# Kernel optimization log

Measured on AMD Instinct MI355X. Metric: run time of the kernel, lower is better.

The kernel has to match this reference:

```python
import jax, jax.numpy as jnp
import numpy as np

D = 1024
H = 16
HD = D // H


def setup_inputs() -> dict:
    key = jax.random.key(0)
    ks = jax.random.split(key, 9)
    s = 1.0 / np.sqrt(D)
    inp = {
        "x": jax.random.normal(ks[0], (2, 2048, D), dtype=jnp.float32),
        "Wq": jax.random.uniform(ks[1], (D, D), jnp.float32, -s, s),
        "bq": jax.random.uniform(ks[2], (D,), jnp.float32, -s, s),
        "Wk": jax.random.uniform(ks[3], (D, D), jnp.float32, -s, s),
        "bk": jax.random.uniform(ks[4], (D,), jnp.float32, -s, s),
        "Wv": jax.random.uniform(ks[5], (D, D), jnp.float32, -s, s),
        "bv": jax.random.uniform(ks[6], (D,), jnp.float32, -s, s),
        "Wo": jax.random.uniform(ks[7], (D, D), jnp.float32, -s, s),
        "bo": jax.random.uniform(ks[8], (D,), jnp.float32, -s, s),
    }
    return inp


def reference(x, Wq, bq, Wk, bk, Wv, bv, Wo, bo):
    B, S, _ = x.shape
    scale = jnp.sqrt(jnp.asarray(HD, dtype=jnp.float32))
    # QKV projections, split into heads: [B, H, S, HD]
    def proj(W, b):
        y = jnp.einsum('bsd,de->bse', x, W) + b
        return y.reshape(B, S, H, HD).transpose(0, 2, 1, 3)
    Q, K, V = proj(Wq, bq), proj(Wk, bk), proj(Wv, bv)
    scores = jnp.einsum('bhqd,bhkd->bhqk', Q, K) / scale  # [B,H,S,S]
    attn = jax.nn.softmax(scores, axis=-1)
    ctx = jnp.einsum('bhqk,bhkd->bhqd', attn, V)
    ctx = ctx.transpose(0, 2, 1, 3).reshape(B, S, D)
    return jnp.einsum('bsd,de->bse', ctx, Wo) + bo
```

## Files before the change

kernel.cpp:

```cpp
#include <hip/hip_runtime.h>
#include <hip/hip_bf16.h>

typedef __attribute__((ext_vector_type(8))) short bf16x8;
typedef __attribute__((ext_vector_type(4))) float f32x4;

constexpr int Sc  = 2048;
constexpr int Dc  = 1024;
constexpr int Hc  = 16;
constexpr int HDc = 64;
constexpr int Mc  = 4096;

constexpr float ECs = 0.18033688011112042f;

__device__ __forceinline__ ushort f2bf(float f) {
  unsigned u = __float_as_uint(f);
  u += 0x7fffu + ((u >> 16) & 1u);
  return (ushort)(u >> 16);
}
__device__ __forceinline__ float bf2f(ushort h) {
  return __uint_as_float(((unsigned)h) << 16);
}

union US8 {
  ushort u[8];
  uint   w[4];
  bf16x8 v;
};

__global__ __launch_bounds__(256) void split_x_kernel(
    const float* __restrict__ X, ushort* __restrict__ H) {
  const int i    = blockIdx.x * 256 + threadIdx.x;
  const float4 v = ((const float4*)X)[i];
  ushort4 h;
  h.x = f2bf(v.x);
  h.y = f2bf(v.y);
  h.z = f2bf(v.z);
  h.w = f2bf(v.w);
  ((ushort4*)H)[i] = h;
}

struct SplitP {
  const float* W[4];
  ushort*      Th[4];
  ushort*      Tl[4];
};

__global__ __launch_bounds__(256) void split_wt_kernel(SplitP p) {
  __shared__ float T[64][69];
  const int z = blockIdx.z;
  const float* W = p.W[z];
  const int t  = threadIdx.x;
  const int c  = (t & 15) * 4;
  const int r  = t >> 4;
  const int n0 = blockIdx.x * 64, k0 = blockIdx.y * 64;
#pragma unroll
  for (int pp = 0; pp < 4; ++pp) {
    const int k    = r + pp * 16;
    const float4 v = *(const float4*)(W + (size_t)(k0 + k) * 1024 + n0 + c);
    T[k][c + 0] = v.x;
    T[k][c + 1] = v.y;
    T[k][c + 2] = v.z;
    T[k][c + 3] = v.w;
  }
  __syncthreads();
#pragma unroll
  for (int pp = 0; pp < 4; ++pp) {
    const int n = r + pp * 16;
    const float x0 = T[c + 0][n], x1 = T[c + 1][n], x2 = T[c + 2][n], x3 = T[c + 3][n];
    ushort4 h, l;
    h.x = f2bf(x0); l.x = f2bf(x0 - bf2f(h.x));
    h.y = f2bf(x1); l.y = f2bf(x1 - bf2f(h.y));
    h.z = f2bf(x2); l.z = f2bf(x2 - bf2f(h.z));
    h.w = f2bf(x3); l.w = f2bf(x3 - bf2f(h.w));
    *(ushort4*)(p.Th[z] + (size_t)(n0 + n) * 1024 + k0 + c) = h;
    *(ushort4*)(p.Tl[z] + (size_t)(n0 + n) * 1024 + k0 + c) = l;
  }
}

struct GemmP {
  const ushort* Bh[3];
  const ushort* Bl[3];
  const float*  bias[3];
  void*         Out[3];
};

template <bool QKV>
__global__ __launch_bounds__(256) void gemm_bf16(
    const ushort* __restrict__ A, GemmP p) {
  __shared__ __align__(16) ushort As[128 * 32];
  __shared__ __align__(16) ushort BsH[128 * 32];
  __shared__ __align__(16) ushort BsL[QKV ? 128 * 32 : 16];

  const int t  = threadIdx.x;
  const int z  = blockIdx.z;
  const int m0 = blockIdx.x * 128, n0 = blockIdx.y * 128;
  const ushort* Bh  = p.Bh[z];
  const ushort* Bl  = p.Bl[z];
  const float* bias = p.bias[z];

  const int lane = t & 63, wave = t >> 6;
  const int wm = (wave & 1) * 64, wn = (wave >> 1) * 64;

  f32x4 acc[4][4];
#pragma unroll
  for (int i = 0; i < 4; ++i)
#pragma unroll
    for (int j = 0; j < 4; ++j) acc[i][j] = (f32x4){0.f, 0.f, 0.f, 0.f};

  const int am = t >> 2;
  const int ac = (t & 3) * 8;
  const ushort* gA  = A  + (size_t)(m0 + am) * 1024 + ac;
  const ushort* gBh = Bh + (size_t)(n0 + am) * 1024 + ac;
  const ushort* gBl = Bl + (size_t)(n0 + am) * 1024 + ac;
  const int l0 = am * 32 + ac, l1 = (am + 64) * 32 + ac;

  const int fr  = lane & 15;
  const int fkb = (lane >> 4) * 16;

  for (int k0 = 0; k0 < 1024; k0 += 32) {
    *(bf16x8*)&As[l0]  = *(const bf16x8*)(gA + k0);
    *(bf16x8*)&As[l1]  = *(const bf16x8*)(gA + k0 + 64 * 1024);
    *(bf16x8*)&BsH[l0] = *(const bf16x8*)(gBh + k0);
    *(bf16x8*)&BsH[l1] = *(const bf16x8*)(gBh + k0 + 64 * 1024);
    if (QKV) {
      *(bf16x8*)&BsL[l0] = *(const bf16x8*)(gBl + k0);
      *(bf16x8*)&BsL[l1] = *(const bf16x8*)(gBl + k0 + 64 * 1024);
    }
    __syncthreads();

    bf16x8 a[4], b_h[4], b_l[4];
#pragma unroll
    for (int i = 0; i < 4; ++i) {
      const int ra = (wm + i * 16 + fr) * 64 + fkb;
      const int rb = (wn + i * 16 + fr) * 64 + fkb;
      a[i]   = *(const bf16x8*)((const char*)As + ra);
      b_h[i] = *(const bf16x8*)((const char*)BsH + rb);
      if (QKV) b_l[i] = *(const bf16x8*)((const char*)BsL + rb);
    }
#pragma unroll
    for (int i = 0; i < 4; ++i)
#pragma unroll
      for (int j = 0; j < 4; ++j) {
        acc[i][j] = __builtin_amdgcn_mfma_f32_16x16x32_bf16(a[i], b_h[j], acc[i][j], 0, 0, 0);
        if (QKV)
          acc[i][j] = __builtin_amdgcn_mfma_f32_16x16x32_bf16(a[i], b_l[j], acc[i][j], 0, 0, 0);
      }
    __syncthreads();
  }

  const float osc = (QKV && z == 0) ? ECs : 1.0f;
  const int cr = (lane >> 4) * 4;
  const int cc = lane & 15;
#pragma unroll
  for (int j = 0; j < 4; ++j) {
    const int n    = n0 + wn + j * 16 + cc;
    const float bv = bias[n];
#pragma unroll
    for (int i = 0; i < 4; ++i) {
      const int mb = m0 + wm + i * 16 + cr;
#pragma unroll
      for (int r = 0; r < 4; ++r) {
        const int m   = mb + r;
        const float v = (acc[i][j][r] + bv) * osc;
        if (QKV) {
          const int b = m >> 11, s = m & 2047, h = n >> 6, hd = n & 63;
          ((ushort*)p.Out[z])[(((size_t)(b * Hc + h) * Sc + s) << 6) + hd] = f2bf(v);
        } else {
          ((float*)p.Out[z])[(size_t)m * 1024 + n] = v;
        }
      }
    }
  }
}

__global__ __launch_bounds__(256) void attn_mfma3(
    const ushort* __restrict__ Q, const ushort* __restrict__ K,
    const ushort* __restrict__ V, ushort* __restrict__ CTX) {
  __shared__ __align__(16) ushort Ks[64 * 72];
  __shared__ __align__(16) ushort Vt[64 * 72];

  const int t    = threadIdx.x;
  const int lane = t & 63, wave = t >> 6;
  const int c16 = lane & 15, quad = lane >> 4;
  const int bh = blockIdx.x, qt = blockIdx.y;
  const int bb = bh >> 4, hh = bh & 15;

  const ushort* Qb = Q + (size_t)bh * Sc * HDc + (size_t)qt * 128 * HDc;
  const ushort* Kb = K + (size_t)bh * Sc * HDc;
  const ushort* Vb = V + (size_t)bh * Sc * HDc;

  bf16x8 aq[2][2];
#pragma unroll
  for (int mt = 0; mt < 2; ++mt)
#pragma unroll
    for (int c = 0; c < 2; ++c)
      aq[mt][c] = *(const bf16x8*)(Qb + (size_t)(wave * 32 + mt * 16 + c16) * 64 + c * 32 + quad * 8);

  US8 ones_u;
#pragma unroll
  for (int e = 0; e < 8; ++e) ones_u.u[e] = 0x3F80;
  const bf16x8 ones = ones_u.v;

  f32x4 ctx[2][4], lacc[2];
#pragma unroll
  for (int mt = 0; mt < 2; ++mt) {
    lacc[mt] = (f32x4){0.f, 0.f, 0.f, 0.f};
#pragma unroll
    for (int j = 0; j < 4; ++j) ctx[mt][j] = (f32x4){0.f, 0.f, 0.f, 0.f};
  }

  const int krow = t >> 2, kc = (t & 3) * 8;
  const int kg = t & 15, dg = t >> 4;
  const int lb = ((kg >> 3) << 5) | ((kg & 3) << 3) | (((kg >> 2) & 1) << 2);

  const ushort* gK = Kb + (size_t)krow * 64 + kc;
  const ushort* gV = Vb + (size_t)(kg * 4) * 64 + dg * 4;

  bf16x8 kr0, kr1;
  ushort4 vr[4];
  kr0 = *(const bf16x8*)(gK);
  kr1 = *(const bf16x8*)(gK + 32);
#pragma unroll
  for (int i = 0; i < 4; ++i) vr[i] = *(const ushort4*)(gV + (size_t)i * 64);

  for (int kt = 0; kt < 32; ++kt) {
    __syncthreads();
    *(bf16x8*)&Ks[krow * 72 + kc]      = kr0;
    *(bf16x8*)&Ks[krow * 72 + kc + 32] = kr1;
    {
      const uint* w0 = (const uint*)&vr[0];
      const uint* w1 = (const uint*)&vr[1];
      const uint* w2 = (const uint*)&vr[2];
      const uint* w3 = (const uint*)&vr[3];
#pragma unroll
      for (int j = 0; j < 4; ++j) {
        const int  wd  = j >> 1;
        const uint sel = (j & 1) ? 0x07060302u : 0x05040100u;
        const uint lo  = __builtin_amdgcn_perm(w1[wd], w0[wd], sel);
        const uint hi  = __builtin_amdgcn_perm(w3[wd], w2[wd], sel);
        *(uint2*)&Vt[(dg * 4 + j) * 72 + lb] = make_uint2(lo, hi);
      }
    }
    __syncthreads();

    if (kt < 31) {
      const size_t adv = (size_t)(kt + 1) * 64 * 64;
      kr0 = *(const bf16x8*)(gK + adv);
      kr1 = *(const bf16x8*)(gK + adv + 32);
#pragma unroll
      for (int i = 0; i < 4; ++i) vr[i] = *(const ushort4*)(gV + adv + (size_t)i * 64);
    }

    f32x4 st[2][4];
#pragma unroll
    for (int mt = 0; mt < 2; ++mt)
#pragma unroll
      for (int j = 0; j < 4; ++j) st[mt][j] = (f32x4){0.f, 0.f, 0.f, 0.f};
#pragma unroll
    for (int c = 0; c < 2; ++c)
#pragma unroll
      for (int j = 0; j < 4; ++j) {
        const bf16x8 ak = *(const bf16x8*)&Ks[(j * 16 + c16) * 72 + c * 32 + quad * 8];
        st[0][j] = __builtin_amdgcn_mfma_f32_16x16x32_bf16(ak, aq[0][c], st[0][j], 0, 0, 0);
        st[1][j] = __builtin_amdgcn_mfma_f32_16x16x32_bf16(ak, aq[1][c], st[1][j], 0, 0, 0);
      }

    US8 pf[2][2];
#pragma unroll
    for (int mt = 0; mt < 2; ++mt)
#pragma unroll
      for (int c2 = 0; c2 < 2; ++c2)
#pragma unroll
        for (int w = 0; w < 4; ++w) {
          const int jj = c2 * 2 + (w >> 1);
          const int r0 = (w & 1) * 2;
          const float pe = __builtin_amdgcn_exp2f(st[mt][jj][r0]);
          const float po = __builtin_amdgcn_exp2f(st[mt][jj][r0 + 1]);
          pf[mt][c2].w[w] = __builtin_amdgcn_perm(
              __float_as_uint(po), __float_as_uint(pe), 0x07060302u);
        }

#pragma unroll
    for (int c2 = 0; c2 < 2; ++c2) {
      lacc[0] = __builtin_amdgcn_mfma_f32_16x16x32_bf16(pf[0][c2].v, ones, lacc[0], 0, 0, 0);
      lacc[1] = __builtin_amdgcn_mfma_f32_16x16x32_bf16(pf[1][c2].v, ones, lacc[1], 0, 0, 0);
#pragma unroll
      for (int j = 0; j < 4; ++j) {
        const bf16x8 bv = *(const bf16x8*)&Vt[(j * 16 + c16) * 72 + c2 * 32 + quad * 8];
        ctx[0][j] = __builtin_amdgcn_mfma_f32_16x16x32_bf16(pf[0][c2].v, bv, ctx[0][j], 0, 0, 0);
        ctx[1][j] = __builtin_amdgcn_mfma_f32_16x16x32_bf16(pf[1][c2].v, bv, ctx[1][j], 0, 0, 0);
      }
    }
  }

#pragma unroll
  for (int mt = 0; mt < 2; ++mt) {
#pragma unroll
    for (int r = 0; r < 4; ++r) {
      const float inv = 1.f / lacc[mt][r];
      const int srow  = qt * 128 + wave * 32 + mt * 16 + quad * 4 + r;
      const size_t rb = ((size_t)(bb * Sc + srow)) * 1024 + hh * 64;
#pragma unroll
      for (int j = 0; j < 4; ++j)
        CTX[rb + j * 16 + c16] = f2bf(ctx[mt][j][r] * inv);
    }
  }
}

extern "C" void kernel_launch(void* const* d_in, const int* in_sizes, int n_in,
                              void* d_out, int out_size, void* d_ws, size_t ws_size,
                              hipStream_t stream) {
  (void)in_sizes; (void)n_in; (void)out_size; (void)ws_size;
  const float* x  = (const float*)d_in[0];
  const float* Wq = (const float*)d_in[1];
  const float* bq = (const float*)d_in[2];
  const float* Wk = (const float*)d_in[3];
  const float* bk = (const float*)d_in[4];
  const float* Wv = (const float*)d_in[5];
  const float* bv = (const float*)d_in[6];
  const float* Wo = (const float*)d_in[7];
  const float* bo = (const float*)d_in[8];

  const size_t MB = 1024 * 1024;
  char* w    = (char*)d_ws;
  ushort* Qw = (ushort*)(w + 0 * MB);
  ushort* Kw = (ushort*)(w + 8 * MB);
  ushort* Vw = (ushort*)(w + 16 * MB);
  ushort* Cw = (ushort*)(w + 24 * MB);
  ushort* Xh = (ushort*)(w + 32 * MB);
  ushort* WT = (ushort*)(w + 40 * MB);
  ushort* Whq = WT + 0 * 1048576; ushort* Wlq = WT + 1 * 1048576;
  ushort* Whk = WT + 2 * 1048576; ushort* Wlk = WT + 3 * 1048576;
  ushort* Whv = WT + 4 * 1048576; ushort* Wlv = WT + 5 * 1048576;
  ushort* Who = WT + 6 * 1048576; ushort* Wlo = WT + 7 * 1048576;

  const dim3 blk(256);

  split_x_kernel<<<4096, blk, 0, stream>>>(x, Xh);

  SplitP sp;
  sp.W[0] = Wq; sp.W[1] = Wk; sp.W[2] = Wv; sp.W[3] = Wo;
  sp.Th[0] = Whq; sp.Th[1] = Whk; sp.Th[2] = Whv; sp.Th[3] = Who;
  sp.Tl[0] = Wlq; sp.Tl[1] = Wlk; sp.Tl[2] = Wlv; sp.Tl[3] = Wlo;
  split_wt_kernel<<<dim3(16, 16, 4), blk, 0, stream>>>(sp);

  GemmP pq;
  pq.Bh[0] = Whq; pq.Bh[1] = Whk; pq.Bh[2] = Whv;
  pq.Bl[0] = Wlq; pq.Bl[1] = Wlk; pq.Bl[2] = Wlv;
  pq.bias[0] = bq; pq.bias[1] = bk; pq.bias[2] = bv;
  pq.Out[0] = Qw; pq.Out[1] = Kw; pq.Out[2] = Vw;
  gemm_bf16<true><<<dim3(Mc / 128, Dc / 128, 3), blk, 0, stream>>>(Xh, pq);

  attn_mfma3<<<dim3(2 * Hc, Sc / 128), blk, 0, stream>>>(Qw, Kw, Vw, Cw);

  GemmP po;
  po.Bh[0] = po.Bh[1] = po.Bh[2] = Who;
  po.Bl[0] = po.Bl[1] = po.Bl[2] = Wlo;
  po.bias[0] = po.bias[1] = po.bias[2] = bo;
  po.Out[0] = po.Out[1] = po.Out[2] = d_out;
  gemm_bf16<false><<<dim3(Mc / 128, Dc / 128, 1), blk, 0, stream>>>(Cw, po);
}
```

Before: 228.9 us.

## Prefetch GEMM tiles into registers and swizzle LDS layout

New measurement: 213.2 us. 1.07x faster.

```diff
diff --git a/kernel.cpp b/kernel.cpp
--- a/kernel.cpp
+++ b/kernel.cpp
@@ -73,7 +73,8 @@
     h.z = f2bf(x2); l.z = f2bf(x2 - bf2f(h.z));
     h.w = f2bf(x3); l.w = f2bf(x3 - bf2f(h.w));
     *(ushort4*)(p.Th[z] + (size_t)(n0 + n) * 1024 + k0 + c) = h;
-    *(ushort4*)(p.Tl[z] + (size_t)(n0 + n) * 1024 + k0 + c) = l;
+    if (z != 3)
+      *(ushort4*)(p.Tl[z] + (size_t)(n0 + n) * 1024 + k0 + c) = l;
   }
 }
 
@@ -108,25 +109,49 @@
     for (int j = 0; j < 4; ++j) acc[i][j] = (f32x4){0.f, 0.f, 0.f, 0.f};
 
   const int am = t >> 2;
-  const int ac = (t & 3) * 8;
-  const ushort* gA  = A  + (size_t)(m0 + am) * 1024 + ac;
-  const ushort* gBh = Bh + (size_t)(n0 + am) * 1024 + ac;
-  const ushort* gBl = Bl + (size_t)(n0 + am) * 1024 + ac;
-  const int l0 = am * 32 + ac, l1 = (am + 64) * 32 + ac;
+  const int ac = t & 3;
+  const ushort* gA  = A  + (size_t)(m0 + am) * 1024 + ac * 8;
+  const ushort* gBh = Bh + (size_t)(n0 + am) * 1024 + ac * 8;
+  const ushort* gBl = Bl + (size_t)(n0 + am) * 1024 + ac * 8;
+  const int sw = ((ac + (am >> 1)) & 3) * 8;
+  const int l0 = am * 32 + sw, l1 = (am + 64) * 32 + sw;
 
   const int fr  = lane & 15;
-  const int fkb = (lane >> 4) * 16;
+  const int fkb = (((lane >> 4) + (fr >> 1)) & 3) * 16;
+
+  bf16x8 rA0, rA1, rH0, rH1, rL0, rL1;
+  rA0 = *(const bf16x8*)(gA);
+  rA1 = *(const bf16x8*)(gA + 64 * 1024);
+  rH0 = *(const bf16x8*)(gBh);
+  rH1 = *(const bf16x8*)(gBh + 64 * 1024);
+  if (QKV) {
+    rL0 = *(const bf16x8*)(gBl);
+    rL1 = *(const bf16x8*)(gBl + 64 * 1024);
+  }
 
   for (int k0 = 0; k0 < 1024; k0 += 32) {
-    *(bf16x8*)&As[l0]  = *(const bf16x8*)(gA + k0);
-    *(bf16x8*)&As[l1]  = *(const bf16x8*)(gA + k0 + 64 * 1024);
-    *(bf16x8*)&BsH[l0] = *(const bf16x8*)(gBh + k0);
-    *(bf16x8*)&BsH[l1] = *(const bf16x8*)(gBh + k0 + 64 * 1024);
+    __syncthreads();
+    *(bf16x8*)&As[l0]  = rA0;
+    *(bf16x8*)&As[l1]  = rA1;
+    *(bf16x8*)&BsH[l0] = rH0;
+    *(bf16x8*)&BsH[l1] = rH1;
     if (QKV) {
-      *(bf16x8*)&BsL[l0] = *(const bf16x8*)(gBl + k0);
-      *(bf16x8*)&BsL[l1] = *(const bf16x8*)(gBl + k0 + 64 * 1024);
+      *(bf16x8*)&BsL[l0] = rL0;
+      *(bf16x8*)&BsL[l1] = rL1;
     }
     __syncthreads();
+
+    if (k0 + 32 < 1024) {
+      const int kn = k0 + 32;
+      rA0 = *(const bf16x8*)(gA + kn);
+      rA1 = *(const bf16x8*)(gA + kn + 64 * 1024);
+      rH0 = *(const bf16x8*)(gBh + kn);
+      rH1 = *(const bf16x8*)(gBh + kn + 64 * 1024);
+      if (QKV) {
+        rL0 = *(const bf16x8*)(gBl + kn);
+        rL1 = *(const bf16x8*)(gBl + kn + 64 * 1024);
+      }
+    }
 
     bf16x8 a[4], b_h[4], b_l[4];
 #pragma unroll
@@ -145,7 +170,6 @@
         if (QKV)
           acc[i][j] = __builtin_amdgcn_mfma_f32_16x16x32_bf16(a[i], b_l[j], acc[i][j], 0, 0, 0);
       }
-    __syncthreads();
   }
 
   const float osc = (QKV && z == 0) ? ECs : 1.0f;
```
